# Performance work log

Hardware: AMD Instinct MI355X
Metric: run time of the kernel (lower is better)

The kernel has to match this reference:

```python
import jax, jax.numpy as jnp
import numpy as np

B, T, F, H = 32768, 64, 8, 16
NUM_LABELS, OUT_WIN = 4, 8
FC1_OUT = F * T          # 512
FC2_OUT = NUM_LABELS * OUT_WIN  # 32


def _lstm_relu(x_tbf, W, U, b):
    """Keras LSTM with activation='relu', recurrent_activation='sigmoid'.
    x_tbf: [T, B, F_in]. Returns all hidden states [T, B, H].
    Gate order in Keras kernel: i, f, c, o."""
    Bv = x_tbf.shape[1]
    h0 = jnp.zeros((Bv, H), x_tbf.dtype)
    c0 = jnp.zeros((Bv, H), x_tbf.dtype)

    def step(carry, xt):
        h, c = carry
        z = xt @ W + h @ U + b  # [B, 4H]
        i, f, g, o = jnp.split(z, 4, axis=-1)
        i = jax.nn.sigmoid(i)
        f = jax.nn.sigmoid(f)
        o = jax.nn.sigmoid(o)
        c = f * c + i * jax.nn.relu(g)
        h = o * jax.nn.relu(c)
        return (h, c), h

    _, hs = jax.lax.scan(step, (h0, c0), x_tbf)
    return hs  # [T, B, H]


def setup_inputs() -> dict:
    key = jax.random.key(0)
    ks = jax.random.split(key, 12)
    s = lambda fan_in: 1.0 / np.sqrt(fan_in)
    x = jax.random.normal(ks[0], (B, T, F), dtype=jnp.float32)
    W1 = jax.random.normal(ks[1], (F, 4 * H), dtype=jnp.float32) * s(F)
    U1 = jax.random.normal(ks[2], (H, 4 * H), dtype=jnp.float32) * s(H)
    b1 = jnp.zeros((4 * H,), jnp.float32)
    W2 = jax.random.normal(ks[3], (H, 4 * H), dtype=jnp.float32) * s(H)
    U2 = jax.random.normal(ks[4], (H, 4 * H), dtype=jnp.float32) * s(H)
    b2 = jnp.zeros((4 * H,), jnp.float32)
    Wfc1 = jax.random.normal(ks[5], (H, FC1_OUT), dtype=jnp.float32) * s(H)
    bfc1 = jnp.zeros((FC1_OUT,), jnp.float32)
    Wfc2 = jax.random.normal(ks[6], (FC1_OUT, FC2_OUT), dtype=jnp.float32) * s(FC1_OUT)
    bfc2 = jnp.zeros((FC2_OUT,), jnp.float32)
    return {"x": x, "W1": W1, "U1": U1, "b1": b1, "W2": W2, "U2": U2,
            "b2": b2, "Wfc1": Wfc1, "bfc1": bfc1, "Wfc2": Wfc2, "bfc2": bfc2}


def reference(x, W1, U1, b1, W2, U2, b2, Wfc1, bfc1, Wfc2, bfc2):
    x_tbf = jnp.transpose(x, (1, 0, 2))        # [T, B, F]
    h1 = _lstm_relu(x_tbf, W1, U1, b1)         # [T, B, H] (return_sequences=True)
    h2 = _lstm_relu(h1, W2, U2, b2)[-1]        # [B, H] (return_sequences=False)
    # Dropout is identity at inference (training=False).
    y = jax.nn.relu(h2 @ Wfc1 + bfc1)          # [B, 512]
    y = y @ Wfc2 + bfc2                        # [B, 32]
    return y
```

## Files before the change

### kernel.cpp

```cpp
#include <hip/hip_runtime.h>
#include <stdint.h>


#define NT 64
#define NF 8

typedef __attribute__((ext_vector_type(8))) short bf16x8;
typedef __attribute__((ext_vector_type(4))) float f32x4;
typedef __attribute__((ext_vector_type(2))) unsigned int u32x2;
typedef __attribute__((ext_vector_type(4))) unsigned int u32x4;

#define MFMA16 __builtin_amdgcn_mfma_f32_16x16x32_bf16

static __device__ __forceinline__ uint32_t bfraw(float f) {
  uint32_t u = __float_as_uint(f);
  return u + 0x7FFFu + ((u >> 16) & 1u);
}
static __device__ __forceinline__ float hipart(uint32_t raw) {
  return __uint_as_float(raw & 0xFFFF0000u);
}
static __device__ __forceinline__ void pack_hl(float a, float b,
                                               uint32_t& hi, uint32_t& lo) {
  uint32_t ra = bfraw(a), rb = bfraw(b);
  hi = (rb & 0xFFFF0000u) | (ra >> 16);
  float la = a - hipart(ra);
  float lb = b - hipart(rb);
  uint32_t rla = bfraw(la), rlb = bfraw(rb == 0u ? 0.f : lb);
  rlb = bfraw(lb);
  lo = (rlb & 0xFFFF0000u) | (rla >> 16);
}
static __device__ __forceinline__ void split_hl(float f, short& hi, short& lo) {
  uint32_t r = bfraw(f);
  hi = (short)(r >> 16);
  float res = f - hipart(r);
  lo = (short)(bfraw(res) >> 16);
}
static __device__ __forceinline__ float sigmoidf_(float v) {
  return __builtin_amdgcn_rcpf(1.0f + __expf(-v));
}
static __device__ __forceinline__ bf16x8 asbf(u32x4 w) {
  union { u32x4 u; bf16x8 b; } c; c.u = w; return c.b;
}
static __device__ __forceinline__ uint32_t bperm(int addr, uint32_t v) {
  return (uint32_t)__builtin_amdgcn_ds_bpermute(addr, (int)v);
}
static __device__ __forceinline__ void lds_fence() {
  asm volatile("s_waitcnt lgkmcnt(0)" ::: "memory");
}

__global__ __launch_bounds__(256, 2) void lstm_fused(
    const float* __restrict__ x,
    const float* __restrict__ W1, const float* __restrict__ U1, const float* __restrict__ b1,
    const float* __restrict__ W2, const float* __restrict__ U2, const float* __restrict__ b2,
    const float* __restrict__ Wfc1, const float* __restrict__ bfc1,
    const float* __restrict__ Wfc2, const float* __restrict__ bfc2,
    float* __restrict__ out)
{
  const int tid  = threadIdx.x;
  const int lane = tid & 63;
  const int wv   = tid >> 6;
  const int col  = lane & 15;
  const int g    = lane >> 4;
  const int base = (blockIdx.x * 4 + wv) * 16;

  __shared__ __align__(16) short cf[4][2][512];
  short* const cfh = &cf[wv][0][0];
  short* const cfl = &cf[wv][1][0];

  bf16x8 B1a[4], B2a[4], B1b[4], B2b[4];
#pragma unroll
  for (int n = 0; n < 4; ++n) {
    const int c = 16 * n + col;
#pragma unroll
    for (int j = 0; j < 8; ++j) {
      const int k = 8 * g + j;
      short h, l;
      if (k < 8)       { split_hl(W1[k * 64 + c], h, l);        B1a[n][j] = h; B2a[n][j] = l; }
      else if (k < 16) { split_hl(W1[(k - 8) * 64 + c], h, l);  B1a[n][j] = h; B2a[n][j] = 0; }
      else             { split_hl(U1[(k - 16) * 64 + c], h, l); B1a[n][j] = h; B2a[n][j] = l; }
      short h2, l2;
      if (k < 16) split_hl(W2[k * 64 + c], h2, l2);
      else        split_hl(U2[(k - 16) * 64 + c], h2, l2);
      B1b[n][j] = h2; B2b[n][j] = l2;
    }
  }

  f32x4 bias1v[4], bias2v[4];
#pragma unroll
  for (int n = 0; n < 4; ++n) {
    bias1v[n] = *(const f32x4*)(b1 + 16 * n + 4 * g);
    bias2v[n] = *(const f32x4*)(b2 + 16 * n + 4 * g);
  }

  const int addrA = ((g & 1) * 32 + col) * 4;
  const int addrB = addrA + 64;

  f32x4 c1 = {0.f, 0.f, 0.f, 0.f};
  f32x4 c2 = {0.f, 0.f, 0.f, 0.f};
  uint32_t h1ph[4] = {0,0,0,0}, h1pl[4] = {0,0,0,0};
  uint32_t h2ph[4] = {0,0,0,0}, h2pl[4] = {0,0,0,0};

  const float* xrow = x + (size_t)(base + col) * (NT * NF);
  f32x4 xa = *(const f32x4*)(xrow);
  f32x4 xb = *(const f32x4*)(xrow + 4);

  for (int i = 0; i < NT; ++i) {
    u32x4 l2b1w, l2b3w;
#pragma unroll
    for (int q = 0; q < 4; ++q) {
      l2b1w[q] = (g < 2) ? h1ph[q] : h2ph[q];
      l2b3w[q] = (g < 2) ? h1pl[q] : h2pl[q];
    }
    uint32_t xh[4], xl[4];
    pack_hl(xa[0], xa[1], xh[0], xl[0]);
    pack_hl(xa[2], xa[3], xh[1], xl[1]);
    pack_hl(xb[0], xb[1], xh[2], xl[2]);
    pack_hl(xb[2], xb[3], xh[3], xl[3]);
    if (i + 1 < NT) {
      xa = *(const f32x4*)(xrow + (i + 1) * NF);
      xb = *(const f32x4*)(xrow + (i + 1) * NF + 4);
    }
    u32x4 l1b1w, l1b3w;
#pragma unroll
    for (int q = 0; q < 4; ++q) {
      uint32_t xw = (g == 0) ? xh[q] : xl[q];
      l1b1w[q] = (g < 2) ? xw : h1ph[q];
      l1b3w[q] = (g < 2) ? 0u : h1pl[q];
    }
    bf16x8 L1B1 = asbf(l1b1w), L1B3 = asbf(l1b3w);
    bf16x8 L2B1 = asbf(l2b1w), L2B3 = asbf(l2b3w);

    f32x4 z[4], y[4];
#pragma unroll
    for (int n = 0; n < 4; ++n) {
      f32x4 zi = MFMA16(B1a[n], L1B1, bias1v[n], 0, 0, 0);
      zi = MFMA16(B2a[n], L1B1, zi, 0, 0, 0);
      zi = MFMA16(B1a[n], L1B3, zi, 0, 0, 0);
      z[n] = zi;
      f32x4 yi = MFMA16(B1b[n], L2B1, bias2v[n], 0, 0, 0);
      yi = MFMA16(B2b[n], L2B1, yi, 0, 0, 0);
      yi = MFMA16(B1b[n], L2B3, yi, 0, 0, 0);
      y[n] = yi;
    }

    f32x4 h1v, h2v;
#pragma unroll
    for (int r = 0; r < 4; ++r) {
      float ig = sigmoidf_(z[0][r]);
      float fg = sigmoidf_(z[1][r]);
      float gg = fmaxf(z[2][r], 0.f);
      float og = sigmoidf_(z[3][r]);
      float cc = fg * c1[r] + ig * gg;
      c1[r] = cc;
      h1v[r] = og * fmaxf(cc, 0.f);
    }
    if (i != 0) {
#pragma unroll
      for (int r = 0; r < 4; ++r) {
        float ig = sigmoidf_(y[0][r]);
        float fg = sigmoidf_(y[1][r]);
        float gg = fmaxf(y[2][r], 0.f);
        float og = sigmoidf_(y[3][r]);
        float cc = fg * c2[r] + ig * gg;
        c2[r] = cc;
        h2v[r] = og * fmaxf(cc, 0.f);
      }
    } else {
      h2v = (f32x4){0.f, 0.f, 0.f, 0.f};
    }

    {
      uint32_t p01h, p01l, p23h, p23l;
      pack_hl(h1v[0], h1v[1], p01h, p01l);
      pack_hl(h1v[2], h1v[3], p23h, p23l);
      h1ph[0] = bperm(addrA, p01h); h1ph[1] = bperm(addrA, p23h);
      h1ph[2] = bperm(addrB, p01h); h1ph[3] = bperm(addrB, p23h);
      h1pl[0] = bperm(addrA, p01l); h1pl[1] = bperm(addrA, p23l);
      h1pl[2] = bperm(addrB, p01l); h1pl[3] = bperm(addrB, p23l);
    }
    {
      uint32_t p01h, p01l, p23h, p23l;
      pack_hl(h2v[0], h2v[1], p01h, p01l);
      pack_hl(h2v[2], h2v[3], p23h, p23l);
      h2ph[0] = bperm(addrA, p01h); h2ph[1] = bperm(addrA, p23h);
      h2ph[2] = bperm(addrB, p01h); h2ph[3] = bperm(addrB, p23h);
      h2pl[0] = bperm(addrA, p01l); h2pl[1] = bperm(addrA, p23l);
      h2pl[2] = bperm(addrB, p01l); h2pl[3] = bperm(addrB, p23l);
    }
  }

  {
    u32x4 b1w, b3w;
#pragma unroll
    for (int q = 0; q < 4; ++q) {
      b1w[q] = (g < 2) ? h1ph[q] : h2ph[q];
      b3w[q] = (g < 2) ? h1pl[q] : h2pl[q];
    }
    bf16x8 L2B1 = asbf(b1w), L2B3 = asbf(b3w);
    f32x4 y[4];
#pragma unroll
    for (int n = 0; n < 4; ++n) {
      f32x4 yi = MFMA16(B1b[n], L2B1, bias2v[n], 0, 0, 0);
      yi = MFMA16(B2b[n], L2B1, yi, 0, 0, 0);
      yi = MFMA16(B1b[n], L2B3, yi, 0, 0, 0);
      y[n] = yi;
    }
    f32x4 h2v;
#pragma unroll
    for (int r = 0; r < 4; ++r) {
      float ig = sigmoidf_(y[0][r]);
      float fg = sigmoidf_(y[1][r]);
      float gg = fmaxf(y[2][r], 0.f);
      float og = sigmoidf_(y[3][r]);
      float cc = fg * c2[r] + ig * gg;
      c2[r] = cc;
      h2v[r] = og * fmaxf(cc, 0.f);
    }
    uint32_t p01h, p01l, p23h, p23l;
    pack_hl(h2v[0], h2v[1], p01h, p01l);
    pack_hl(h2v[2], h2v[3], p23h, p23l);
    h2ph[0] = bperm(addrA, p01h); h2ph[1] = bperm(addrA, p23h);
    h2ph[2] = bperm(addrB, p01h); h2ph[3] = bperm(addrB, p23h);
    h2pl[0] = bperm(addrA, p01l); h2pl[1] = bperm(addrA, p23l);
    h2pl[2] = bperm(addrB, p01l); h2pl[3] = bperm(addrB, p23l);
  }

  u32x4 bwf;
#pragma unroll
  for (int q = 0; q < 4; ++q) bwf[q] = (g < 2) ? h2ph[q] : h2pl[q];
  bf16x8 Bfc = asbf(bwf);

  f32x4 acc2[2];
#pragma unroll
  for (int nn = 0; nn < 2; ++nn)
    acc2[nn] = *(const f32x4*)(bfc2 + 16 * nn + 4 * g);

  for (int kc = 0; kc < 16; ++kc) {
#pragma unroll
    for (int t = 0; t < 2; ++t) {
      const int mt = 2 * kc + t;
      bf16x8 A1h, A1l;
#pragma unroll
      for (int j = 0; j < 8; ++j) {
        float w = Wfc1[((8 * g + j) & 15) * 512 + 16 * mt + col];
        short h, l; split_hl(w, h, l);
        A1h[j] = h; A1l[j] = l;
      }
      f32x4 bv = *(const f32x4*)(bfc1 + 16 * mt + 4 * g);
      f32x4 acc = MFMA16(A1h, Bfc, bv, 0, 0, 0);
      acc = MFMA16(A1l, Bfc, acc, 0, 0, 0);
      uint32_t q01h, q01l, q23h, q23l;
      pack_hl(fmaxf(acc[0], 0.f), fmaxf(acc[1], 0.f), q01h, q01l);
      pack_hl(fmaxf(acc[2], 0.f), fmaxf(acc[3], 0.f), q23h, q23l);
      *(u32x2*)((char*)cfh + col * 64 + 32 * t + 8 * g) = (u32x2){q01h, q23h};
      *(u32x2*)((char*)cfl + col * 64 + 32 * t + 8 * g) = (u32x2){q01l, q23l};
    }
    lds_fence();
    bf16x8 Bh = *(const bf16x8*)((char*)cfh + col * 64 + 16 * g);
    bf16x8 Bl = *(const bf16x8*)((char*)cfl + col * 64 + 16 * g);
#pragma unroll
    for (int nn = 0; nn < 2; ++nn) {
      bf16x8 A2h, A2l;
#pragma unroll
      for (int j = 0; j < 8; ++j) {
        float w = Wfc2[(size_t)(32 * kc + 8 * g + j) * 32 + 16 * nn + col];
        short h, l; split_hl(w, h, l);
        A2h[j] = h; A2l[j] = l;
      }
      acc2[nn] = MFMA16(A2h, Bh, acc2[nn], 0, 0, 0);
      acc2[nn] = MFMA16(A2h, Bl, acc2[nn], 0, 0, 0);
      acc2[nn] = MFMA16(A2l, Bh, acc2[nn], 0, 0, 0);
    }
    lds_fence();
  }

#pragma unroll
  for (int nn = 0; nn < 2; ++nn)
    *(f32x4*)(out + (size_t)(base + col) * 32 + 16 * nn + 4 * g) = acc2[nn];
}

extern "C" void kernel_launch(void* const* d_in, const int* in_sizes, int n_in,
                              void* d_out, int out_size, void* d_ws, size_t ws_size,
                              hipStream_t stream) {
  const float* x    = (const float*)d_in[0];
  const float* W1   = (const float*)d_in[1];
  const float* U1   = (const float*)d_in[2];
  const float* b1   = (const float*)d_in[3];
  const float* W2   = (const float*)d_in[4];
  const float* U2   = (const float*)d_in[5];
  const float* b2   = (const float*)d_in[6];
  const float* Wfc1 = (const float*)d_in[7];
  const float* bfc1 = (const float*)d_in[8];
  const float* Wfc2 = (const float*)d_in[9];
  const float* bfc2 = (const float*)d_in[10];

  lstm_fused<<<dim3(512), dim3(256), 0, stream>>>(
      x, W1, U1, b1, W2, U2, b2, Wfc1, bfc1, Wfc2, bfc2, (float*)d_out);
}
```

Before: 235.7 us.

## Use hardware bf16 pack conversion, pad LDS rows, and issue h1 permutes earlier

Replaces the manual round-to-nearest bf16 bit manipulation with the v_cvt_pk_bf16_f32 instruction for hi/lo splitting. It also pads the per-wave LDS staging rows from 64 to 80 bytes to reduce bank conflicts. Finally, it moves the layer-1 hidden-state pack and bpermute ahead of the layer-2 gate math so LDS permute latency can overlap with computation. The hardware conversion may differ slightly in rounding for NaN and denormal inputs, and padding adds a little shared memory.

```diff
diff --git a/kernel.cpp b/kernel.cpp
--- a/kernel.cpp
+++ b/kernel.cpp
@@ -12,28 +12,24 @@
 
 #define MFMA16 __builtin_amdgcn_mfma_f32_16x16x32_bf16
 
-static __device__ __forceinline__ uint32_t bfraw(float f) {
-  uint32_t u = __float_as_uint(f);
-  return u + 0x7FFFu + ((u >> 16) & 1u);
-}
-static __device__ __forceinline__ float hipart(uint32_t raw) {
-  return __uint_as_float(raw & 0xFFFF0000u);
+static __device__ __forceinline__ uint32_t cvt_pk(float a, float b) {
+  uint32_t r;
+  asm("v_cvt_pk_bf16_f32 %0, %1, %2" : "=v"(r) : "v"(a), "v"(b));
+  return r;
 }
 static __device__ __forceinline__ void pack_hl(float a, float b,
                                                uint32_t& hi, uint32_t& lo) {
-  uint32_t ra = bfraw(a), rb = bfraw(b);
-  hi = (rb & 0xFFFF0000u) | (ra >> 16);
-  float la = a - hipart(ra);
-  float lb = b - hipart(rb);
-  uint32_t rla = bfraw(la), rlb = bfraw(rb == 0u ? 0.f : lb);
-  rlb = bfraw(lb);
-  lo = (rlb & 0xFFFF0000u) | (rla >> 16);
+  hi = cvt_pk(a, b);
+  float ha = __uint_as_float(hi << 16);
+  float hb = __uint_as_float(hi & 0xFFFF0000u);
+  lo = cvt_pk(a - ha, b - hb);
 }
 static __device__ __forceinline__ void split_hl(float f, short& hi, short& lo) {
-  uint32_t r = bfraw(f);
-  hi = (short)(r >> 16);
-  float res = f - hipart(r);
-  lo = (short)(bfraw(res) >> 16);
+  uint32_t w = cvt_pk(f, 0.f);
+  hi = (short)(w & 0xFFFFu);
+  float hf = __uint_as_float(w << 16);
+  uint32_t wl = cvt_pk(f - hf, 0.f);
+  lo = (short)(wl & 0xFFFFu);
 }
 static __device__ __forceinline__ float sigmoidf_(float v) {
   return __builtin_amdgcn_rcpf(1.0f + __expf(-v));
@@ -63,9 +59,9 @@
   const int g    = lane >> 4;
   const int base = (blockIdx.x * 4 + wv) * 16;
 
-  __shared__ __align__(16) short cf[4][2][512];
-  short* const cfh = &cf[wv][0][0];
-  short* const cfl = &cf[wv][1][0];
+  __shared__ __align__(16) char cf[4][2][16 * 80];
+  char* const cfh = &cf[wv][0][0];
+  char* const cfl = &cf[wv][1][0];
 
   bf16x8 B1a[4], B2a[4], B1b[4], B2b[4];
 #pragma unroll
@@ -143,7 +139,7 @@
       y[n] = yi;
     }
 
-    f32x4 h1v, h2v;
+    f32x4 h1v;
 #pragma unroll
     for (int r = 0; r < 4; ++r) {
       float ig = sigmoidf_(z[0][r]);
@@ -154,6 +150,17 @@
       c1[r] = cc;
       h1v[r] = og * fmaxf(cc, 0.f);
     }
+    {
+      uint32_t p01h, p01l, p23h, p23l;
+      pack_hl(h1v[0], h1v[1], p01h, p01l);
+      pack_hl(h1v[2], h1v[3], p23h, p23l);
+      h1ph[0] = bperm(addrA, p01h); h1ph[1] = bperm(addrA, p23h);
+      h1ph[2] = bperm(addrB, p01h); h1ph[3] = bperm(addrB, p23h);
+      h1pl[0] = bperm(addrA, p01l); h1pl[1] = bperm(addrA, p23l);
+      h1pl[2] = bperm(addrB, p01l); h1pl[3] = bperm(addrB, p23l);
+    }
+
+    f32x4 h2v;
     if (i != 0) {
 #pragma unroll
       for (int r = 0; r < 4; ++r) {
@@ -168,16 +175,6 @@
     } else {
       h2v = (f32x4){0.f, 0.f, 0.f, 0.f};
     }
-
-    {
-      uint32_t p01h, p01l, p23h, p23l;
-      pack_hl(h1v[0], h1v[1], p01h, p01l);
-      pack_hl(h1v[2], h1v[3], p23h, p23l);
-      h1ph[0] = bperm(addrA, p01h); h1ph[1] = bperm(addrA, p23h);
-      h1ph[2] = bperm(addrB, p01h); h1ph[3] = bperm(addrB, p23h);
-      h1pl[0] = bperm(addrA, p01l); h1pl[1] = bperm(addrA, p23l);
-      h1pl[2] = bperm(addrB, p01l); h1pl[3] = bperm(addrB, p23l);
-    }
     {
       uint32_t p01h, p01l, p23h, p23l;
       pack_hl(h2v[0], h2v[1], p01h, p01l);
@@ -252,12 +249,12 @@
       uint32_t q01h, q01l, q23h, q23l;
       pack_hl(fmaxf(acc[0], 0.f), fmaxf(acc[1], 0.f), q01h, q01l);
       pack_hl(fmaxf(acc[2], 0.f), fmaxf(acc[3], 0.f), q23h, q23l);
-      *(u32x2*)((char*)cfh + col * 64 + 32 * t + 8 * g) = (u32x2){q01h, q23h};
-      *(u32x2*)((char*)cfl + col * 64 + 32 * t + 8 * g) = (u32x2){q01l, q23l};
+      *(u32x2*)(cfh + col * 80 + 32 * t + 8 * g) = (u32x2){q01h, q23h};
+      *(u32x2*)(cfl + col * 80 + 32 * t + 8 * g) = (u32x2){q01l, q23l};
     }
     lds_fence();
-    bf16x8 Bh = *(const bf16x8*)((char*)cfh + col * 64 + 16 * g);
-    bf16x8 Bl = *(const bf16x8*)((char*)cfl + col * 64 + 16 * g);
+    bf16x8 Bh = *(const bf16x8*)(cfh + col * 80 + 16 * g);
+    bf16x8 Bl = *(const bf16x8*)(cfl + col * 80 + 16 * g);
 #pragma unroll
     for (int nn = 0; nn < 2; ++nn) {
       bf16x8 A2h, A2l;
```

New measurement: 219.8 us. 1.07x faster.
